# Kernel tuning notes

Hardware: AMD Instinct MI355X
Metric: run time of the kernel (lower is better)

## Reference

```python
import jax, jax.numpy as jnp
import numpy as np

EPS = 1e-12  # torch F.normalize eps


def setup_inputs() -> dict:
    key = jax.random.key(0)
    k1, k2, k3 = jax.random.split(key, 3)
    N, C, H, W = 64, 512, 30, 30
    K = 64
    x = jax.random.normal(k1, (N, C, H, W), dtype=jnp.float32)
    conv_w = jax.random.normal(k2, (K, C), dtype=jnp.float32) * 0.02
    centroids = jax.random.uniform(k3, (K, C), dtype=jnp.float32)
    return {"x": x, "conv_w": conv_w, "centroids": centroids}


def reference(x, conv_w, centroids):
    N, C, H, W = x.shape
    K = conv_w.shape[0]
    # descriptor-wise L2 normalization over channel dim (torch F.normalize, p=2, dim=1)
    norm = jnp.sqrt(jnp.sum(x * x, axis=1, keepdims=True))
    x = x / jnp.maximum(norm, EPS)
    xf = x.reshape(N, C, H * W)  # [N, C, P]
    # 1x1 conv (no bias) -> logits [N, K, P]; softmax over clusters K
    logits = jnp.einsum("ncp,kc->nkp", xf, conv_w)
    a = jax.nn.softmax(logits, axis=1)  # [N, K, P]
    # vlad[n,k,c] = sum_p a[n,k,p] * (x[n,c,p] - centroids[k,c])
    #            = (a @ x^T)[n,k,c] - centroids[k,c] * sum_p a[n,k,p]
    vlad = jnp.einsum("nkp,ncp->nkc", a, xf) - a.sum(axis=-1)[:, :, None] * centroids[None]
    return vlad
```

## Files before the change

### kernel.cpp

```cpp
#include <hip/hip_runtime.h>

typedef __attribute__((ext_vector_type(8))) __bf16 bf16x8;
typedef __attribute__((ext_vector_type(4))) __bf16 bf16x4;
typedef __attribute__((ext_vector_type(4))) float f32x4;

#define LGKM_BAR() do { asm volatile("s_waitcnt lgkmcnt(0)" ::: "memory"); \
                        __builtin_amdgcn_s_barrier(); } while (0)

namespace {
constexpr int N_ = 64, C_ = 512, P_ = 900, K_ = 64;
constexpr int PP = 960;
constexpr size_t TOT_X = (size_t)N_ * C_ * P_;
constexpr size_t AT_BYTES = (size_t)N_ * K_ * PP * 2;
constexpr size_t ASUM_OFF = AT_BYTES;
constexpr size_t WB_OFF   = ASUM_OFF + (size_t)N_ * K_ * 4;
}

__global__ __launch_bounds__(256) void k_prep_w(const float* __restrict__ w,
                                                __bf16* __restrict__ wb,
                                                float* __restrict__ asum) {
  const int t = blockIdx.x * 256 + threadIdx.x;
  const int i = t * 4;
  if (i < K_ * C_) {
    float4 v = *reinterpret_cast<const float4*>(w + i);
    wb[i]   = (__bf16)v.x; wb[i+1] = (__bf16)v.y;
    wb[i+2] = (__bf16)v.z; wb[i+3] = (__bf16)v.w;
  }
  if (t < N_ * K_) asum[t] = 0.f;
}

__global__ __launch_bounds__(256) void k_phase1(const float* __restrict__ x,
                                                const __bf16* __restrict__ wb,
                                                __bf16* __restrict__ at,
                                                float* __restrict__ asum) {
  const int n   = blockIdx.y;
  const int tid = threadIdx.x;
  const int w   = tid >> 6, l = tid & 63;
  const int l15 = l & 15,  lh = l >> 4;
  const int p   = blockIdx.x * 64 + w * 16 + l15;
  const int pc  = p < P_ ? p : P_ - 1;
  const float*  xp    = x + (size_t)n * C_ * P_ + (size_t)lh * 8 * P_ + pc;
  const __bf16* wbase = wb + (size_t)l15 * C_ + lh * 8;

  f32x4 acc[4] = {};
  float sq = 0.f;
  #pragma unroll
  for (int s = 0; s < 16; ++s) {
    float g[8];
    #pragma unroll
    for (int j = 0; j < 8; ++j)
      g[j] = xp[(size_t)(s * 32 + j) * P_];
    bf16x8 b;
    #pragma unroll
    for (int j = 0; j < 8; ++j) { sq = fmaf(g[j], g[j], sq); b[j] = (__bf16)g[j]; }
    #pragma unroll
    for (int m = 0; m < 4; ++m) {
      bf16x8 a = *reinterpret_cast<const bf16x8*>(wbase + (size_t)m * 16 * C_ + s * 32);
      acc[m] = __builtin_amdgcn_mfma_f32_16x16x32_bf16(a, b, acc[m], 0, 0, 0);
    }
  }
  sq += __shfl_xor(sq, 16, 64);
  sq += __shfl_xor(sq, 32, 64);
  const float invn = 1.f / fmaxf(sqrtf(sq), 1e-12f);
  const bool  valid = p < P_;

  float ps = 0.f;
  #pragma unroll
  for (int m = 0; m < 4; ++m)
    #pragma unroll
    for (int r = 0; r < 4; ++r) {
      acc[m][r] = __expf(acc[m][r] * invn);
      ps += acc[m][r];
    }
  ps += __shfl_xor(ps, 16, 64);
  ps += __shfl_xor(ps, 32, 64);
  const float invs = 1.f / ps;
  const float sc   = invs * invn;

  #pragma unroll
  for (int m = 0; m < 4; ++m)
    #pragma unroll
    for (int r = 0; r < 4; ++r) {
      const int k = 16 * m + lh * 4 + r;
      at[((size_t)n * K_ + k) * PP + p] =
          valid ? (__bf16)(acc[m][r] * sc) : (__bf16)0.f;
    }
  #pragma unroll
  for (int m = 0; m < 4; ++m)
    #pragma unroll
    for (int r = 0; r < 4; ++r) {
      float v = valid ? acc[m][r] * invs : 0.f;
      v += __shfl_xor(v, 1, 64); v += __shfl_xor(v, 2, 64);
      v += __shfl_xor(v, 4, 64); v += __shfl_xor(v, 8, 64);
      if (l15 == 0)
        unsafeAtomicAdd(asum + n * K_ + 16 * m + lh * 4 + r, v);
    }
}

__global__ __launch_bounds__(256) void k_phase2(const float* __restrict__ x,
                                                const __bf16* __restrict__ at,
                                                const float* __restrict__ asum,
                                                const float* __restrict__ cent,
                                                float* __restrict__ out) {
  __shared__ __bf16 Al[2][64][40];
  __shared__ __bf16 Xl[2][64][40];
  const int n   = blockIdx.y;
  const int c0  = blockIdx.x * 64;
  const int tid = threadIdx.x;
  const int w   = tid >> 6, l = tid & 63;
  const int l15 = l & 15,  lh = l >> 4;

  const int ak  = tid >> 2, ach = tid & 3;
  const int xc  = tid >> 3, xch = tid & 7;
  const size_t abase  = ((size_t)n * K_ + ak) * PP + ach * 8;
  const size_t xbase0 = ((size_t)n * C_ + c0 + xc) * P_ + xch * 4;
  const size_t xbase1 = ((size_t)n * C_ + c0 + xc + 32) * P_ + xch * 4;

  f32x4 acc[4] = {};
  bf16x8 na; float4 v0, v1;

  auto LOAD = [&](int s) {
    na = *reinterpret_cast<const bf16x8*>(at + abase + s * 32);
    size_t o0 = xbase0 + s * 32; if (o0 > TOT_X - 4) o0 = TOT_X - 4;
    size_t o1 = xbase1 + s * 32; if (o1 > TOT_X - 4) o1 = TOT_X - 4;
    v0 = *reinterpret_cast<const float4*>(x + o0);
    v1 = *reinterpret_cast<const float4*>(x + o1);
  };
  auto STORE = [&](int b) {
    *reinterpret_cast<bf16x8*>(&Al[b][ak][ach * 8]) = na;
    bf16x4 p0 = { (__bf16)v0.x, (__bf16)v0.y, (__bf16)v0.z, (__bf16)v0.w };
    bf16x4 p1 = { (__bf16)v1.x, (__bf16)v1.y, (__bf16)v1.z, (__bf16)v1.w };
    *reinterpret_cast<bf16x4*>(&Xl[b][xc][xch * 4])      = p0;
    *reinterpret_cast<bf16x4*>(&Xl[b][xc + 32][xch * 4]) = p1;
  };

  LOAD(0); STORE(0);
  LGKM_BAR();

  #pragma unroll 2
  for (int s = 0; s < 29; ++s) {
    if (s < 28) LOAD(s + 1);
    bf16x8 b = *reinterpret_cast<const bf16x8*>(&Xl[s & 1][16 * w + l15][lh * 8]);
    #pragma unroll
    for (int m = 0; m < 4; ++m) {
      bf16x8 a = *reinterpret_cast<const bf16x8*>(&Al[s & 1][16 * m + l15][lh * 8]);
      acc[m] = __builtin_amdgcn_mfma_f32_16x16x32_bf16(a, b, acc[m], 0, 0, 0);
    }
    if (s < 28) STORE((s + 1) & 1);
    LGKM_BAR();
  }

  const int c = c0 + 16 * w + l15;
  #pragma unroll
  for (int m = 0; m < 4; ++m) {
    #pragma unroll
    for (int r = 0; r < 4; ++r) {
      const int k = 16 * m + lh * 4 + r;
      out[((size_t)n * K_ + k) * C_ + c] =
          acc[m][r] - asum[n * K_ + k] * cent[(size_t)k * C_ + c];
    }
  }
}

extern "C" void kernel_launch(void* const* d_in, const int* in_sizes, int n_in,
                              void* d_out, int out_size, void* d_ws, size_t ws_size,
                              hipStream_t stream) {
  const float* x    = (const float*)d_in[0];
  const float* w    = (const float*)d_in[1];
  const float* cent = (const float*)d_in[2];
  float* out = (float*)d_out;
  char* wsb  = (char*)d_ws;
  __bf16* at   = (__bf16*)wsb;
  float*  asum = (float*)(wsb + ASUM_OFF);
  __bf16* wb   = (__bf16*)(wsb + WB_OFF);

  k_prep_w<<<dim3(32), dim3(256), 0, stream>>>(w, wb, asum);
  k_phase1<<<dim3(15, 64), dim3(256), 0, stream>>>(x, wb, at, asum);
  k_phase2<<<dim3(8, 64), dim3(256), 0, stream>>>(x, at, asum, cent, out);
}
```

Before: 83.54 us.

## Stage weights in LDS and prefetch x loads with deeper register pipeline in phase1

The bf16 conv weights are written in an interleaved layout matching the MFMA A-fragment, so phase1 can load the whole 64x512 weight into shared memory once per block instead of reading it from global memory on every step. Blocks grow to 512 threads covering 128 pixels, which halves the number of blocks that must each stage the weights. The x loads are software-pipelined six steps ahead in registers to hide global latency. In exchange the kernel uses 64KB of LDS and more registers, which limits occupancy, and the final pixel tile now runs partially idle.

```diff
diff --git a/kernel.cpp b/kernel.cpp
--- a/kernel.cpp
+++ b/kernel.cpp
@@ -13,52 +13,74 @@
 constexpr size_t TOT_X = (size_t)N_ * C_ * P_;
 constexpr size_t AT_BYTES = (size_t)N_ * K_ * PP * 2;
 constexpr size_t ASUM_OFF = AT_BYTES;
-constexpr size_t WB_OFF   = ASUM_OFF + (size_t)N_ * K_ * 4;
+constexpr size_t WBR_OFF  = ASUM_OFF + (size_t)N_ * K_ * 4;
 }
 
 __global__ __launch_bounds__(256) void k_prep_w(const float* __restrict__ w,
-                                                __bf16* __restrict__ wb,
+                                                __bf16* __restrict__ wbr,
                                                 float* __restrict__ asum) {
-  const int t = blockIdx.x * 256 + threadIdx.x;
-  const int i = t * 4;
-  if (i < K_ * C_) {
-    float4 v = *reinterpret_cast<const float4*>(w + i);
-    wb[i]   = (__bf16)v.x; wb[i+1] = (__bf16)v.y;
-    wb[i+2] = (__bf16)v.z; wb[i+3] = (__bf16)v.w;
-  }
-  if (t < N_ * K_) asum[t] = 0.f;
-}
-
-__global__ __launch_bounds__(256) void k_phase1(const float* __restrict__ x,
-                                                const __bf16* __restrict__ wb,
+  const int T = blockIdx.x * 256 + threadIdx.x;
+  const int k = T >> 6, oct = T & 63;
+  const float4 a = *reinterpret_cast<const float4*>(w + (size_t)k * C_ + oct * 8);
+  const float4 b = *reinterpret_cast<const float4*>(w + (size_t)k * C_ + oct * 8 + 4);
+  bf16x8 o = { (__bf16)a.x, (__bf16)a.y, (__bf16)a.z, (__bf16)a.w,
+               (__bf16)b.x, (__bf16)b.y, (__bf16)b.z, (__bf16)b.w };
+  *reinterpret_cast<bf16x8*>(wbr + ((size_t)oct * K_ + k) * 8) = o;
+  asum[T] = 0.f;
+}
+
+__global__ __launch_bounds__(512) void k_phase1(const float* __restrict__ x,
+                                                const __bf16* __restrict__ wbr,
                                                 __bf16* __restrict__ at,
                                                 float* __restrict__ asum) {
+  __shared__ bf16x8 Wl[4096];
   const int n   = blockIdx.y;
   const int tid = threadIdx.x;
   const int w   = tid >> 6, l = tid & 63;
   const int l15 = l & 15,  lh = l >> 4;
-  const int p   = blockIdx.x * 64 + w * 16 + l15;
+  const int p   = blockIdx.x * 128 + w * 16 + l15;
   const int pc  = p < P_ ? p : P_ - 1;
-  const float*  xp    = x + (size_t)n * C_ * P_ + (size_t)lh * 8 * P_ + pc;
-  const __bf16* wbase = wb + (size_t)l15 * C_ + lh * 8;
+  const float* xp = x + (size_t)n * C_ * P_ + (size_t)lh * 8 * P_ + pc;
+
+  bf16x8 tmp[8];
+  #pragma unroll
+  for (int it = 0; it < 8; ++it)
+    tmp[it] = *reinterpret_cast<const bf16x8*>(wbr + (size_t)(it * 512 + tid) * 8);
+
+  float g[6][8];
+  #pragma unroll
+  for (int b = 0; b < 6; ++b)
+    #pragma unroll
+    for (int j = 0; j < 8; ++j)
+      g[b][j] = xp[(size_t)(b * 32 + j) * P_];
+
+  #pragma unroll
+  for (int it = 0; it < 8; ++it)
+    Wl[it * 512 + tid] = tmp[it];
+  LGKM_BAR();
 
   f32x4 acc[4] = {};
   float sq = 0.f;
   #pragma unroll
   for (int s = 0; s < 16; ++s) {
-    float g[8];
-    #pragma unroll
-    for (int j = 0; j < 8; ++j)
-      g[j] = xp[(size_t)(s * 32 + j) * P_];
     bf16x8 b;
     #pragma unroll
-    for (int j = 0; j < 8; ++j) { sq = fmaf(g[j], g[j], sq); b[j] = (__bf16)g[j]; }
+    for (int j = 0; j < 8; ++j) {
+      const float v = g[s % 6][j];
+      sq = fmaf(v, v, sq); b[j] = (__bf16)v;
+    }
+    if (s + 6 < 16) {
+      #pragma unroll
+      for (int j = 0; j < 8; ++j)
+        g[s % 6][j] = xp[(size_t)((s + 6) * 32 + j) * P_];
+    }
     #pragma unroll
     for (int m = 0; m < 4; ++m) {
-      bf16x8 a = *reinterpret_cast<const bf16x8*>(wbase + (size_t)m * 16 * C_ + s * 32);
+      bf16x8 a = Wl[(s * 4 + lh) * 64 + 16 * m + l15];
       acc[m] = __builtin_amdgcn_mfma_f32_16x16x32_bf16(a, b, acc[m], 0, 0, 0);
     }
   }
+
   sq += __shfl_xor(sq, 16, 64);
   sq += __shfl_xor(sq, 32, 64);
   const float invn = 1.f / fmaxf(sqrtf(sq), 1e-12f);
@@ -77,14 +99,16 @@
   const float invs = 1.f / ps;
   const float sc   = invs * invn;
 
-  #pragma unroll
-  for (int m = 0; m < 4; ++m)
-    #pragma unroll
-    for (int r = 0; r < 4; ++r) {
-      const int k = 16 * m + lh * 4 + r;
-      at[((size_t)n * K_ + k) * PP + p] =
-          valid ? (__bf16)(acc[m][r] * sc) : (__bf16)0.f;
-    }
+  if (p < PP) {
+    #pragma unroll
+    for (int m = 0; m < 4; ++m)
+      #pragma unroll
+      for (int r = 0; r < 4; ++r) {
+        const int k = 16 * m + lh * 4 + r;
+        at[((size_t)n * K_ + k) * PP + p] =
+            valid ? (__bf16)(acc[m][r] * sc) : (__bf16)0.f;
+      }
+  }
   #pragma unroll
   for (int m = 0; m < 4; ++m)
     #pragma unroll
@@ -172,9 +196,9 @@
   char* wsb  = (char*)d_ws;
   __bf16* at   = (__bf16*)wsb;
   float*  asum = (float*)(wsb + ASUM_OFF);
-  __bf16* wb   = (__bf16*)(wsb + WB_OFF);
-
-  k_prep_w<<<dim3(32), dim3(256), 0, stream>>>(w, wb, asum);
-  k_phase1<<<dim3(15, 64), dim3(256), 0, stream>>>(x, wb, at, asum);
+  __bf16* wbr  = (__bf16*)(wsb + WBR_OFF);
+
+  k_prep_w<<<dim3(16), dim3(256), 0, stream>>>(w, wbr, asum);
+  k_phase1<<<dim3(8, 64), dim3(512), 0, stream>>>(x, wbr, at, asum);
   k_phase2<<<dim3(8, 64), dim3(256), 0, stream>>>(x, at, asum, cent, out);
 }
```

Measured after the change: 69.82 us. -16.4%, faster.
